# Optimization experiments

Hardware: AMD Instinct MI355X
Metric: run time of the kernel (lower is better)

The kernel has to match this reference:

```python
import jax, jax.numpy as jnp
import numpy as np

B, S, D = 2, 1024, 512
E, K = 8, 2          # num_experts, top_k (hardcoded in EncoderLayerMOE)
HMOE = 4             # SMoE_MHA heads
HD = D // HMOE       # 128 head dim for local experts
HID = 4 * D          # 2048 expert hidden (both extractors)
AH = 4               # attention heads
DK = D // AH
NEG = -1e9


def layer_norm(x, w, b, eps=1e-12):
    mu = x.mean(-1, keepdims=True)
    var = ((x - mu) ** 2).mean(-1, keepdims=True)
    return (x - mu) * jax.lax.rsqrt(var + eps) * w + b


def moe(x, gate_w, gate_b, w1, b1, w2, b2):
    """Dense all-expert SMoE, gather top-k, re-softmax topk weights (faithful).
    x: [..., d]; w1: [E,d,H]; w2: [E,H,d]."""
    gate_scores = x @ gate_w + gate_b                      # [..., E]
    sm = jax.nn.softmax(gate_scores, axis=-1)
    topk_s, topk_i = jax.lax.top_k(sm, K)                  # [..., K]
    h1 = jax.nn.relu(jnp.einsum('...d,edh->...eh', x, w1) + b1)   # [..., E, H]
    out = jnp.einsum('...eh,ehd->...ed', h1, w2) + b2      # [..., E, d]
    idx = jnp.broadcast_to(topk_i[..., None], topk_i.shape + (out.shape[-1],))
    sel = jnp.take_along_axis(out, idx, axis=-2)           # [..., K, d]
    w = jax.nn.softmax(topk_s, axis=-1)[..., None]         # re-softmax of topk scores
    return (sel * w).sum(-2)


def local_extractor(x, pre_w, pre_b, gate_w, gate_b, w1, b1, w2, b2, align_w, align_b):
    b, s, d = x.shape
    xp = x @ pre_w + pre_b
    xf = xp.reshape(b, s, HMOE, HD).transpose(0, 2, 1, 3)  # [b,h,s,hd]
    eo = moe(xf, gate_w, gate_b, w1, b1, w2, b2)
    xf = xf + eo
    xo = xf.transpose(0, 2, 1, 3).reshape(b, s, d)
    return xo @ align_w + align_b


def mha(xq, xkv, mask, wq, bq, wk, bk, wv, bv, wo, bo):
    b, sq, d = xq.shape
    sk = xkv.shape[1]
    q = (xq @ wq + bq).reshape(b, sq, AH, DK).transpose(0, 2, 1, 3)
    k = (xkv @ wk + bk).reshape(b, sk, AH, DK).transpose(0, 2, 1, 3)
    v = (xkv @ wv + bv).reshape(b, sk, AH, DK).transpose(0, 2, 1, 3)
    scores = jnp.einsum('bhqd,bhkd->bhqk', q, k) / jnp.sqrt(jnp.float32(DK))
    m = mask[:, None, :, :]                                 # [b,1,1,sk]
    scores = jnp.where(m, scores, NEG)
    attn = jax.nn.softmax(scores, axis=-1)
    attn = jnp.where(m, attn, 0.0)
    o = jnp.einsum('bhqk,bhkd->bhqd', attn, v)
    o = o.transpose(0, 2, 1, 3).reshape(b, sq, d)
    return o @ wo + bo


def setup_inputs() -> dict:
    key = jax.random.key(0)
    ks = iter(jax.random.split(key, 64))
    def p(shape, scale=0.02):
        return (jax.random.normal(next(ks), shape, jnp.float32) * scale)
    z = lambda *s: jnp.zeros(s, jnp.float32)
    o = lambda *s: jnp.ones(s, jnp.float32)
    return dict(
        x=jax.random.normal(next(ks), (B, S, D), jnp.float32),
        pre_w=p((D, D)), pre_b=z(D),
        l_gate_w=p((HD, E)), l_gate_b=z(E),
        l_w1=p((E, HD, HID)), l_b1=z(E, HID),
        l_w2=p((E, HID, HD)), l_b2=z(E, HD),
        align_w=p((D, D)), align_b=z(D),
        ln1_w=o(D), ln1_b=z(D),
        wq=p((D, D)), bq=z(D), wk=p((D, D)), bk=z(D),
        wv=p((D, D)), bv=z(D), wo=p((D, D)), bo=z(D),
        ln2_w=o(D), ln2_b=z(D),
        g_gate_w=p((D, E)), g_gate_b=z(E),
        g_w1=p((E, D, HID)), g_b1=z(E, HID),
        g_w2=p((E, HID, D)), g_b2=z(E, D),
        mask=jnp.ones((B, 1, S), bool),
    )


def reference(x, pre_w, pre_b, l_gate_w, l_gate_b, l_w1, l_b1, l_w2, l_b2,
              align_w, align_b, ln1_w, ln1_b, wq, bq, wk, bk, wv, bv, wo, bo,
              ln2_w, ln2_b, g_gate_w, g_gate_b, g_w1, g_b1, g_w2, g_b2, mask):
    # EncoderLayerMOE.forward, eval mode, normalize_before=True, cache=None
    residual = x
    xl = local_extractor(x, pre_w, pre_b, l_gate_w, l_gate_b,
                         l_w1, l_b1, l_w2, l_b2, align_w, align_b)
    xn = layer_norm(xl, ln1_w, ln1_b)
    att = mha(xn, xn, mask, wq, bq, wk, bk, wv, bv, wo, bo)
    x1 = residual + att
    residual = x1
    x2 = layer_norm(x1, ln2_w, ln2_b)
    g = moe(x2, g_gate_w, g_gate_b, g_w1, g_b1, g_w2, g_b2)
    out = residual + g
    return out
```

## Files before the change

kernel.cpp:

```cpp
#include <hip/hip_runtime.h>

typedef unsigned short ushort_t;
typedef __attribute__((ext_vector_type(8))) short short8;
typedef __attribute__((ext_vector_type(4))) short short4v;
typedef __attribute__((ext_vector_type(4))) float f32x4;

constexpr int B_    = 2;
constexpr int S_    = 1024;
constexpr int D_    = 512;
constexpr int E_    = 8;
constexpr int HMOE_ = 4;
constexpr int HD_   = 128;
constexpr int HID_  = 2048;
constexpr int AH_   = 4;
constexpr int NTOK  = B_ * S_;
constexpr int NSUB  = B_ * HMOE_ * S_;

#define DEVINL __device__ __forceinline__

DEVINL ushort_t f2bf(float f) {
    union { float f; unsigned int i; } c;
    c.f = f;
    unsigned int x = c.i;
    return (ushort_t)((x + 0x7fffu + ((x >> 16) & 1u)) >> 16);
// ... 296 lines not shown
    #pragma unroll
    for (int j = 0; j < 16; j++) {
        int cc = rl * 16 + j;
        dst[(size_t)cc * R + cl] = f2bf(tile[cl][cc]);
    }
}

struct WCItem { const float* src; ushort_t* dst; int R, C, nbx, nby, start; };
struct WCAll  { WCItem it[10]; };

__global__ __launch_bounds__(256) void wconv_all_k(WCAll a)
{
    __shared__ float tile[64][65];
    const int bidx = blockIdx.x;
    int i = 0;
    #pragma unroll
    for (int j = 1; j < 10; j++) if (bidx >= a.it[j].start) i = j;
    const WCItem wit = a.it[i];
    const int local = bidx - wit.start;
    const int bx = local % wit.nbx;
    const int rest = local / wit.nbx;
    const int by = rest % wit.nby;
    const int e  = rest / wit.nby;
    const int R = wit.R, C = wit.C;
    const int c0 = bx * 64, r0 = by * 64;
    const float* src = wit.src + ((size_t)e * R + r0) * C + c0;
    const int cl = threadIdx.x & 63, rl = threadIdx.x >> 6;
    #pragma unroll
    for (int j = 0; j < 16; j++) {
        int rr = rl * 16 + j;
        tile[rr][cl] = src[(size_t)rr * C + cl];
    }
    __syncthreads();
    ushort_t* dst = wit.dst + ((size_t)e * C + c0) * R + r0;
    #pragma unroll
    for (int j = 0; j < 16; j++) {
        int cc = rl * 16 + j;
        dst[(size_t)cc * R + cl] = f2bf(tile[cl][cc]);
    }
}

__global__ __launch_bounds__(256) void vtrans_bf_k(
    const ushort_t* __restrict__ Vbf, ushort_t* __restrict__ VT)
{
    __shared__ ushort_t tile[64][68];
    const int s0 = blockIdx.x * 64;
    const int d0 = blockIdx.y * 64;
    const int bh = blockIdx.z;
    const int b = bh >> 2, h = bh & 3;
    const ushort_t* src = Vbf + (size_t)(b * S_ + s0) * D_ + h * HD_ + d0;
    const int cl = threadIdx.x & 63, rl = threadIdx.x >> 6;
    #pragma unroll
    for (int j = 0; j < 16; j++) {
        int rr = rl * 16 + j;
        tile[rr][cl] = src[(size_t)rr * D_ + cl];
    }
    __syncthreads();
    ushort_t* dst = VT + ((size_t)bh * HD_ + d0) * S_ + s0;
    #pragma unroll
    for (int j = 0; j < 16; j++) {
        int cc = rl * 16 + j;
        dst[(size_t)cc * S_ + cl] = tile[cl][cc];
    }
}

template <bool LOCAL>
__global__ __launch_bounds__(256) void gate_score_k(
    const float* __restrict__ X, const float* __restrict__ gwm,
    const float* __restrict__ gb, int2* __restrict__ choice,
    float2* __restrict__ cweight)
{
    constexpr int DIMD = LOCAL ? HD_ : D_;
    constexpr int PL = DIMD / 64;
    const int t = blockIdx.x * 4 + (threadIdx.x >> 6);
    const int lane = threadIdx.x & 63;
    const float* x = X + (LOCAL ? local_off(t) : (size_t)t * D_);
    float xr[PL];
    #pragma unroll
    for (int i = 0; i < PL; i++) xr[i] = x[lane + 64 * i];
    float sc[8];
    #pragma unroll
    for (int e = 0; e < 8; e++) {
        float a = 0.f;
        #pragma unroll
        for (int i = 0; i < PL; i++)
            a = fmaf(xr[i], gwm[(size_t)(lane + 64 * i) * E_ + e], a);
        #pragma unroll
        for (int o2 = 32; o2; o2 >>= 1) a += __shfl_xor(a, o2);
        sc[e] = a;
    }
    if (lane == 0) {
        float mx = -1e30f;
        #pragma unroll
        for (int e = 0; e < 8; e++) { sc[e] += gb[e]; mx = fmaxf(mx, sc[e]); }
        float p[8], psum = 0.f;
        #pragma unroll
        for (int e = 0; e < 8; e++) { p[e] = expf(sc[e] - mx); psum += p[e]; }
        float inv = 1.f / psum;
        #pragma unroll
        for (int e = 0; e < 8; e++) p[e] *= inv;
        int i0 = 0;
        for (int e = 1; e < 8; e++) if (p[e] > p[i0]) i0 = e;
        int i1 = (i0 == 0) ? 1 : 0;
        for (int e = 0; e < 8; e++) if (e != i0 && p[e] > p[i1]) i1 = e;
        float e0 = expf(p[i0]), e1 = expf(p[i1]);
        float wnorm = 1.f / (e0 + e1);
        choice[t]  = (int2){i0, i1};
        cweight[t] = (float2){e0 * wnorm, e1 * wnorm};
    }
}

template <int CAP>
__global__ __launch_bounds__(256) void gate_build_k(
    const int2* __restrict__ choice, const float2* __restrict__ cweight,
    int* __restrict__ cnt, int* __restrict__ idx, float* __restrict__ gwv)
{
    __shared__ int wtot[4];
    __shared__ int basesh;
    const int e = blockIdx.x;
    const int tid = threadIdx.x;
    const int lane = tid & 63, wv = tid >> 6;
    if (tid == 0) basesh = 0;
    __syncthreads();
    for (int t0 = 0; t0 < CAP; t0 += 256) {
        int t = t0 + tid;
        int2 ch = choice[t];
        float2 cw = cweight[t];
        bool m0 = (ch.x == e);
        bool m = m0 | (ch.y == e);
        float w = m0 ? cw.x : cw.y;
        unsigned long long mask = __ballot(m);
        int posw = __popcll(mask & ((1ull << lane) - 1ull));
        if (lane == 0) wtot[wv] = __popcll(mask);
        __syncthreads();
        int base = basesh;
        int woff = 0, tot = 0;
        #pragma unroll
        for (int i = 0; i < 4; i++) {
            int c = wtot[i];
            tot += c;
            if (i < wv) woff += c;
        }
        if (m) {
            int p = base + woff + posw;
            idx[e * CAP + p] = t;
            gwv[e * CAP + p] = w;
        }
        __syncthreads();
        if (tid == 0) basesh = base + tot;
    }
    __syncthreads();
    int total = basesh;
    if (tid == 0) cnt[e] = total;
    int padEnd = (total + 63) & ~63;
    if (padEnd > CAP) padEnd = CAP;
    for (int p = total + tid; p < padEnd; p += 256) {
        idx[e * CAP + p] = 0;
        gwv[e * CAP + p] = 0.f;
    }
}

template <int DIMD, int GSPLIT>
__global__ __launch_bounds__(256, 3) void ffn_grouped3_k(
    const ushort_t* __restrict__ Xbf,
    const ushort_t* __restrict__ w1t, const float* __restrict__ b1,
    const ushort_t* __restrict__ w2t, const float* __restrict__ b2,
    const int* __restrict__ cnt, const int* __restrict__ idx,
    const float* __restrict__ gwv, float* __restrict__ OUT)
{
    constexpr int K1  = DIMD;
    constexpr int NT2 = DIMD / 128;
    constexpr int CAP = (DIMD == HD_) ? NSUB : NTOK;
    constexpr int HC  = 128;
    constexpr int CHUNKS = HID_ / HC / GSPLIT;
    constexpr bool PIPE = (NT2 == 1);

    __shared__ ushort_t bufA[64 * 72];
    __shared__ ushort_t bufB[128 * 72];
    __shared__ ushort_t Hs[64 * 136];
    __shared__ float    gws[64];
    __shared__ size_t   toffs[64];

    const int tid  = threadIdx.x;
    const int lane = tid & 63;
    const int wv   = tid >> 6;
    const int e    = blockIdx.x & 7;
    const int rest = blockIdx.x >> 3;
    const int mt   = rest / GSPLIT;
    const int g    = rest % GSPLIT;
    const int m0   = mt * 64;

    if (m0 >= cnt[e]) return;

    if (tid < 64) {
        int t = idx[e * CAP + m0 + tid];
        toffs[tid] = (DIMD == HD_) ? local_off(t) : (size_t)t * D_;
        gws[tid]   = gwv[e * CAP + m0 + tid];
    }
    __syncthreads();

    const int l15 = lane & 15, l4 = lane >> 4;
    const int ar = tid >> 2, as = (tid & 3) * 16;
    const int bn = tid >> 1, bs = (tid & 1) * 32;

    f32x4 accO[NT2][4][2];
    #pragma unroll
    for (int n2 = 0; n2 < NT2; n2++)
        #pragma unroll
        for (int mi = 0; mi < 4; mi++)
            #pragma unroll
            for (int ni = 0; ni < 2; ni++)
                accO[n2][mi][ni] = (f32x4){0.f, 0.f, 0.f, 0.f};

    const ushort_t* w1e = w1t + (size_t)e * HID_ * K1;
    const ushort_t* w2e = w2t + (size_t)e * DIMD * HID_;
    const float* b1e = b1 + (size_t)e * HID_;

    short8 ra0, ra1, rb0, rb1, rb2, rb3;

    const int hc0 = g * CHUNKS * HC;
    for (int hc = hc0; hc < hc0 + CHUNKS * HC; hc += HC) {
        f32x4 acc1[4][2];
        #pragma unroll
        for (int mi = 0; mi < 4; mi++)
            #pragma unroll
            for (int ni = 0; ni < 2; ni++)
                acc1[mi][ni] = (f32x4){0.f, 0.f, 0.f, 0.f};

        if (PIPE) {
            const ushort_t* xp = Xbf + toffs[ar] + as;
            ra0 = *reinterpret_cast<const short8*>(xp);
            ra1 = *reinterpret_cast<const short8*>(xp + 8);
            const ushort_t* wp = w1e + (size_t)(hc + bn) * K1 + bs;
            rb0 = *reinterpret_cast<const short8*>(wp);
            rb1 = *reinterpret_cast<const short8*>(wp + 8);
            rb2 = *reinterpret_cast<const short8*>(wp + 16);
            rb3 = *reinterpret_cast<const short8*>(wp + 24);
        }

        for (int k0 = 0; k0 < K1; k0 += 64) {
            __syncthreads();
            if (PIPE) {
                ushort_t* dst = &bufA[ar * 72 + as];
                *reinterpret_cast<short8*>(dst)     = ra0;
                *reinterpret_cast<short8*>(dst + 8) = ra1;
                ushort_t* dstb = &bufB[bn * 72 + bs];
                *reinterpret_cast<short8*>(dstb)      = rb0;
                *reinterpret_cast<short8*>(dstb + 8)  = rb1;
                *reinterpret_cast<short8*>(dstb + 16) = rb2;
                *reinterpret_cast<short8*>(dstb + 24) = rb3;
                if (k0 + 64 < K1) {
                    const ushort_t* xp = Xbf + toffs[ar] + k0 + 64 + as;
                    ra0 = *reinterpret_cast<const short8*>(xp);
                    ra1 = *reinterpret_cast<const short8*>(xp + 8);
                    const ushort_t* wp = w1e + (size_t)(hc + bn) * K1 + k0 + 64 + bs;
                    rb0 = *reinterpret_cast<const short8*>(wp);
                    rb1 = *reinterpret_cast<const short8*>(wp + 8);
                    rb2 = *reinterpret_cast<const short8*>(wp + 16);
                    rb3 = *reinterpret_cast<const short8*>(wp + 24);
                }
            } else {
                {
                    const ushort_t* xp = Xbf + toffs[ar] + k0 + as;
                    ushort_t* dst = &bufA[ar * 72 + as];
                    *reinterpret_cast<short8*>(dst)     = *reinterpret_cast<const short8*>(xp);
                    *reinterpret_cast<short8*>(dst + 8) = *reinterpret_cast<const short8*>(xp + 8);
                }
                {
                    const ushort_t* wp = w1e + (size_t)(hc + bn) * K1 + k0 + bs;
                    ushort_t* dst = &bufB[bn * 72 + bs];
                    #pragma unroll
                    for (int j = 0; j < 32; j += 8)
                        *reinterpret_cast<short8*>(dst + j) = *reinterpret_cast<const short8*>(wp + j);
                }
            }
            __syncthreads();
            #pragma unroll
            for (int ks = 0; ks < 2; ks++) {
                short8 af[4], bfr[2];
                #pragma unroll
                for (int mi = 0; mi < 4; mi++)
                    af[mi] = *reinterpret_cast<const short8*>(&bufA[(mi * 16 + l15) * 72 + ks * 32 + l4 * 8]);
                #pragma unroll
                for (int ni = 0; ni < 2; ni++)
                    bfr[ni] = *reinterpret_cast<const short8*>(&bufB[(wv * 32 + ni * 16 + l15) * 72 + ks * 32 + l4 * 8]);
                #pragma unroll
                for (int mi = 0; mi < 4; mi++)
                    #pragma unroll
                    for (int ni = 0; ni < 2; ni++)
                        acc1[mi][ni] = __builtin_amdgcn_mfma_f32_16x16x32_bf16(
                            af[mi], bfr[ni], acc1[mi][ni], 0, 0, 0);
            }
        }

        if (PIPE) {
            const ushort_t* wp = w2e + (size_t)bn * HID_ + hc + bs;
            rb0 = *reinterpret_cast<const short8*>(wp);
            rb1 = *reinterpret_cast<const short8*>(wp + 8);
            rb2 = *reinterpret_cast<const short8*>(wp + 16);
            rb3 = *reinterpret_cast<const short8*>(wp + 24);
        }

        float b1v0 = b1e[hc + wv * 32 + l15];
        float b1v1 = b1e[hc + wv * 32 + 16 + l15];
        #pragma unroll
        for (int mi = 0; mi < 4; mi++)
            #pragma unroll
            for (int ni = 0; ni < 2; ni++) {
                float bb = (ni == 0) ? b1v0 : b1v1;
                #pragma unroll
                for (int r = 0; r < 4; r++) {
                    int row = mi * 16 + l4 * 4 + r;
                    int col = wv * 32 + ni * 16 + l15;
                    Hs[row * 136 + col] = f2bf(fmaxf(acc1[mi][ni][r] + bb, 0.f));
                }
            }

        #pragma unroll
        for (int n2 = 0; n2 < NT2; n2++) {
            #pragma unroll
            for (int k2t = 0; k2t < 2; k2t++) {
                __syncthreads();
                if (PIPE) {
                    ushort_t* dst = &bufB[bn * 72 + bs];
                    *reinterpret_cast<short8*>(dst)      = rb0;
                    *reinterpret_cast<short8*>(dst + 8)  = rb1;
                    *reinterpret_cast<short8*>(dst + 16) = rb2;
                    *reinterpret_cast<short8*>(dst + 24) = rb3;
                    if (!(n2 == NT2 - 1 && k2t == 1)) {
                        int nn2 = (k2t == 1) ? n2 + 1 : n2;
                        int nk  = (k2t == 1) ? 0 : 1;
                        const ushort_t* wp = w2e + (size_t)(nn2 * 128 + bn) * HID_ + hc + nk * 64 + bs;
                        rb0 = *reinterpret_cast<const short8*>(wp);
                        rb1 = *reinterpret_cast<const short8*>(wp + 8);
                        rb2 = *reinterpret_cast<const short8*>(wp + 16);
                        rb3 = *reinterpret_cast<const short8*>(wp + 24);
                    }
                } else {
                    const ushort_t* wp = w2e + (size_t)(n2 * 128 + bn) * HID_ + hc + k2t * 64 + bs;
                    ushort_t* dst = &bufB[bn * 72 + bs];
                    #pragma unroll
                    for (int j = 0; j < 32; j += 8)
                        *reinterpret_cast<short8*>(dst + j) = *reinterpret_cast<const short8*>(wp + j);
                }
                __syncthreads();
                #pragma unroll
                for (int ks = 0; ks < 2; ks++) {
                    short8 af[4], bfr[2];
                    #pragma unroll
                    for (int mi = 0; mi < 4; mi++)
                        af[mi] = *reinterpret_cast<const short8*>(&Hs[(mi * 16 + l15) * 136 + k2t * 64 + ks * 32 + l4 * 8]);
                    #pragma unroll
                    for (int ni = 0; ni < 2; ni++)
                        bfr[ni] = *reinterpret_cast<const short8*>(&bufB[(wv * 32 + ni * 16 + l15) * 72 + ks * 32 + l4 * 8]);
                    #pragma unroll
                    for (int mi = 0; mi < 4; mi++)
                        #pragma unroll
                        for (int ni = 0; ni < 2; ni++)
                            accO[n2][mi][ni] = __builtin_amdgcn_mfma_f32_16x16x32_bf16(
                                af[mi], bfr[ni], accO[n2][mi][ni], 0, 0, 0);
                }
            }
        }
    }

    #pragma unroll
    for (int n2 = 0; n2 < NT2; n2++) {
        float b2v0 = (g == 0) ? b2[(size_t)e * DIMD + n2 * 128 + wv * 32 + l15] : 0.f;
        float b2v1 = (g == 0) ? b2[(size_t)e * DIMD + n2 * 128 + wv * 32 + 16 + l15] : 0.f;
        #pragma unroll
        for (int mi = 0; mi < 4; mi++)
            #pragma unroll
            for (int r = 0; r < 4; r++) {
                int row = mi * 16 + l4 * 4 + r;
                float gg = gws[row];
                if (gg != 0.f) {
                    float* op = OUT + toffs[row] + n2 * 128 + wv * 32;
                    atomicAdd(op + l15,      gg * (accO[n2][mi][0][r] + b2v0));
                    atomicAdd(op + 16 + l15, gg * (accO[n2][mi][1][r] + b2v1));
                }
            }
    }
}

__global__ __launch_bounds__(256) void ffn1g_k(
    const ushort_t* __restrict__ Xbf,
    const ushort_t* __restrict__ w1t, const float* __restrict__ b1,
    const int* __restrict__ cnt, const int* __restrict__ idx,
    int hbase, ushort_t* __restrict__ Hbuf)
{
    __shared__ ushort_t bufA[64 * 72];
    __shared__ ushort_t bufB[128 * 72];
    __shared__ size_t   toffs[64];
    __shared__ int      sbase;

    const int tid  = threadIdx.x;
    const int lane = tid & 63;
    const int wv   = tid >> 6;
    const int e    = blockIdx.x & 7;
    const int rest = blockIdx.x >> 3;
    const int mt   = rest >> 3;
    const int hs   = rest & 7;
    const int m0   = mt * 64;
    const int ce   = cnt[e];
    if (m0 >= ce) return;

    if (tid < 64) toffs[tid] = (size_t)idx[e * NTOK + m0 + tid] * D_;
    if (tid == 0) {
        int s = 0;
        for (int j = 0; j < e; j++) s += cnt[j];
        sbase = s;
    }
    __syncthreads();

    const int l15 = lane & 15, l4 = lane >> 4;
    const int ar = tid >> 2, as = (tid & 3) * 16;
    const int bn = tid >> 1, bs = (tid & 1) * 32;
    const int hc = hbase + hs * 128;

    const ushort_t* w1e = w1t + (size_t)e * HID_ * D_;

    f32x4 acc1[4][2];
    #pragma unroll
    for (int mi = 0; mi < 4; mi++)
        #pragma unroll
        for (int ni = 0; ni < 2; ni++)
            acc1[mi][ni] = (f32x4){0.f, 0.f, 0.f, 0.f};

    short8 ra0, ra1, rb0, rb1, rb2, rb3;
    {
        const ushort_t* xp = Xbf + toffs[ar] + as;
        ra0 = *reinterpret_cast<const short8*>(xp);
        ra1 = *reinterpret_cast<const short8*>(xp + 8);
        const ushort_t* wp = w1e + (size_t)(hc + bn) * D_ + bs;
        rb0 = *reinterpret_cast<const short8*>(wp);
        rb1 = *reinterpret_cast<const short8*>(wp + 8);
        rb2 = *reinterpret_cast<const short8*>(wp + 16);
        rb3 = *reinterpret_cast<const short8*>(wp + 24);
    }
    for (int k0 = 0; k0 < D_; k0 += 64) {
        __syncthreads();
        {
            ushort_t* dst = &bufA[ar * 72 + as];
            *reinterpret_cast<short8*>(dst)     = ra0;
            *reinterpret_cast<short8*>(dst + 8) = ra1;
            ushort_t* dstb = &bufB[bn * 72 + bs];
            *reinterpret_cast<short8*>(dstb)      = rb0;
            *reinterpret_cast<short8*>(dstb + 8)  = rb1;
            *reinterpret_cast<short8*>(dstb + 16) = rb2;
            *reinterpret_cast<short8*>(dstb + 24) = rb3;
        }
        if (k0 + 64 < D_) {
            const ushort_t* xp = Xbf + toffs[ar] + k0 + 64 + as;
            ra0 = *reinterpret_cast<const short8*>(xp);
            ra1 = *reinterpret_cast<const short8*>(xp + 8);
            const ushort_t* wp = w1e + (size_t)(hc + bn) * D_ + k0 + 64 + bs;
            rb0 = *reinterpret_cast<const short8*>(wp);
            rb1 = *reinterpret_cast<const short8*>(wp + 8);
            rb2 = *reinterpret_cast<const short8*>(wp + 16);
            rb3 = *reinterpret_cast<const short8*>(wp + 24);
        }
        __syncthreads();
        #pragma unroll
        for (int ks = 0; ks < 2; ks++) {
            short8 af[4], bfr[2];
            #pragma unroll
            for (int mi = 0; mi < 4; mi++)
                af[mi] = *reinterpret_cast<const short8*>(&bufA[(mi * 16 + l15) * 72 + ks * 32 + l4 * 8]);
            #pragma unroll
            for (int ni = 0; ni < 2; ni++)
                bfr[ni] = *reinterpret_cast<const short8*>(&bufB[(wv * 32 + ni * 16 + l15) * 72 + ks * 32 + l4 * 8]);
            #pragma unroll
            for (int mi = 0; mi < 4; mi++)
                #pragma unroll
                for (int ni = 0; ni < 2; ni++)
                    acc1[mi][ni] = __builtin_amdgcn_mfma_f32_16x16x32_bf16(
                        af[mi], bfr[ni], acc1[mi][ni], 0, 0, 0);
        }
    }

    const int slotbase = sbase + m0;
    const int hout = (hc - hbase);
    float b1v0 = b1[(size_t)e * HID_ + hc + wv * 32 + l15];
    float b1v1 = b1[(size_t)e * HID_ + hc + wv * 32 + 16 + l15];
    #pragma unroll
    for (int mi = 0; mi < 4; mi++)
        #pragma unroll
        for (int ni = 0; ni < 2; ni++) {
            float bb = (ni == 0) ? b1v0 : b1v1;
            #pragma unroll
            for (int r = 0; r < 4; r++) {
                int row = mi * 16 + l4 * 4 + r;
                if (m0 + row < ce) {
                    int col = hout + wv * 32 + ni * 16 + l15;
                    Hbuf[(size_t)(slotbase + row) * 1024 + col] =
                        f2bf(fmaxf(acc1[mi][ni][r] + bb, 0.f));
                }
            }
        }
}

template <bool ADD_B2>
__global__ __launch_bounds__(256) void ffn2g_k(
    const ushort_t* __restrict__ Hbuf,
    const ushort_t* __restrict__ w2t, const float* __restrict__ b2,
    const int* __restrict__ cnt, const int* __restrict__ idx,
    const float* __restrict__ gwv, int hbase, float* __restrict__ OUT)
{
    __shared__ ushort_t bufA[32 * 72];
    __shared__ ushort_t bufB[128 * 72];
    __shared__ float    gws[32];
    __shared__ size_t   toffs[32];
    __shared__ int      sbase;

    const int tid  = threadIdx.x;
    const int lane = tid & 63;
    const int wv   = tid >> 6;
    const int e    = blockIdx.x & 7;
    const int rest = blockIdx.x >> 3;
    const int mt   = rest >> 2;
    const int n2   = rest & 3;
    const int m0   = mt * 32;
    const int ce   = cnt[e];
    if (m0 >= ce) return;

    if (tid < 32) {
        toffs[tid] = (size_t)idx[e * NTOK + m0 + tid] * D_;
        gws[tid]   = gwv[e * NTOK + m0 + tid];
    }
    if (tid == 0) {
        int s = 0;
        for (int j = 0; j < e; j++) s += cnt[j];
        sbase = s;
    }
    __syncthreads();
// ... 469 lines not shown
            sum += __shfl_xor(sum, 1);
            sum += __shfl_xor(sum, 2);
            sum += __shfl_xor(sum, 4);
            if ((tid & 7) == 0) { mrow[r] = mnew; lrow[r] = lrow[r] * alpha + sum; arow[r] = alpha; }
        }
        __syncthreads();

        {
            #pragma unroll
            for (int i2 = 0; i2 < 4; i2++) {
                float al = arow[py * 4 + i2];
                #pragma unroll
                for (int j = 0; j < 4; j++) o[i2][j] *= al;
            }
            #pragma unroll 4
            for (int k = 0; k < KC; k++) {
                float4 pv = *reinterpret_cast<const float4*>(&psT[k][py * 4]);
                float4 vv = *reinterpret_cast<const float4*>(V + base + (size_t)(kc + k) * D_ + px * 4);
                float pa[4] = {pv.x, pv.y, pv.z, pv.w};
                #pragma unroll
                for (int i2 = 0; i2 < 4; i2++) {
                    o[i2][0] = fmaf(pa[i2], vv.x, o[i2][0]);
                    o[i2][1] = fmaf(pa[i2], vv.y, o[i2][1]);
                    o[i2][2] = fmaf(pa[i2], vv.z, o[i2][2]);
                    o[i2][3] = fmaf(pa[i2], vv.w, o[i2][3]);
                }
            }
        }
        __syncthreads();
    }

    #pragma unroll
    for (int i2 = 0; i2 < 4; i2++) {
        float inv = 1.f / lrow[py * 4 + i2];
        float4 ov;
        ov.x = o[i2][0] * inv; ov.y = o[i2][1] * inv;
        ov.z = o[i2][2] * inv; ov.w = o[i2][3] * inv;
        *reinterpret_cast<float4*>(AO + base + (size_t)(q0 + py * 4 + i2) * D_ + px * 4) = ov;
    }
}

__global__ __launch_bounds__(256) void copy_out_k(
    const float* __restrict__ X, float* __restrict__ Y, int n)
{
    int base = (blockIdx.x * 256 + threadIdx.x) * 4;
    if (base < n)
        *reinterpret_cast<float4*>(Y + base) = *reinterpret_cast<const float4*>(X + base);
}

extern "C" void kernel_launch(void* const* d_in, const int* in_sizes, int n_in,
                              void* d_out, int out_size, void* d_ws, size_t ws_size,
                              hipStream_t stream)
{
    (void)in_sizes; (void)n_in; (void)out_size;
    const float* x        = (const float*)d_in[0];
    const float* pre_w    = (const float*)d_in[1];
    const float* pre_b    = (const float*)d_in[2];
    const float* l_gate_w = (const float*)d_in[3];
    const float* l_gate_b = (const float*)d_in[4];
    const float* l_w1     = (const float*)d_in[5];
    const float* l_b1     = (const float*)d_in[6];
    const float* l_w2     = (const float*)d_in[7];
    const float* l_b2     = (const float*)d_in[8];
    const float* align_w  = (const float*)d_in[9];
    const float* align_b  = (const float*)d_in[10];
    const float* ln1_w    = (const float*)d_in[11];
    const float* ln1_b    = (const float*)d_in[12];
    const float* wq       = (const float*)d_in[13];
    const float* bq       = (const float*)d_in[14];
    const float* wk       = (const float*)d_in[15];
    const float* bk       = (const float*)d_in[16];
    const float* wv       = (const float*)d_in[17];
    const float* bv       = (const float*)d_in[18];
    const float* wo       = (const float*)d_in[19];
    const float* bo       = (const float*)d_in[20];
    const float* ln2_w    = (const float*)d_in[21];
    const float* ln2_b    = (const float*)d_in[22];
    const float* g_gate_w = (const float*)d_in[23];
    const float* g_gate_b = (const float*)d_in[24];
    const float* g_w1     = (const float*)d_in[25];
    const float* g_b1     = (const float*)d_in[26];
    const float* g_w2     = (const float*)d_in[27];
    const float* g_b2     = (const float*)d_in[28];

    char* ws = (char*)d_ws;
    const size_t MB  = 1024 * 1024;
    const size_t MB4 = (size_t)NTOK * D_ * sizeof(float);
    float* W0 = (float*)(ws + 0 * MB);
    float* W1 = (float*)(ws + 4 * MB);
    float* W2 = (float*)(ws + 8 * MB);

    const bool pre = ws_size >= (size_t)59 * MB;

    char* blob = ws + (pre ? 12 : 16) * MB;
    int*    cntl = (int*)(blob);
    int*    cntg = (int*)(blob + 32);
    int*    idxl = (int*)(blob + 64);
    int*    idxg = (int*)(blob + 64 + 262144);
    float*  gwvl = (float*)(blob + 64 + 262144 + 65536);
    float*  gwvg = (float*)(blob + 64 + 262144 + 65536 + 262144);
    int2*   chl  = (int2*)(blob + 64 + 262144 + 65536 + 262144 + 65536);
    float2* cwl  = (float2*)((char*)chl + 65536);
    int2*   chg  = (int2*)((char*)cwl + 65536);
    float2* cwg  = (float2*)((char*)chg + 16384);

    ushort_t* preT   = (ushort_t*)(ws + 14 * MB);
    ushort_t* alignT = (ushort_t*)(ws + 14 * MB + 512 * 1024);
    ushort_t* wqT    = (ushort_t*)(ws + 15 * MB);
    ushort_t* wkT    = (ushort_t*)(ws + 15 * MB + 512 * 1024);
    ushort_t* wvT    = (ushort_t*)(ws + 16 * MB);
    ushort_t* woT    = (ushort_t*)(ws + 16 * MB + 512 * 1024);
    ushort_t* XBF  = (ushort_t*)(ws + 17 * MB);
    ushort_t* Vbf  = (ushort_t*)(ws + 4 * MB);
    ushort_t* VTb  = (ushort_t*)(ws + 6 * MB);
    ushort_t* Qbf  = (ushort_t*)(ws + 8 * MB);
    ushort_t* Kbf  = (ushort_t*)(ws + 10 * MB);
    ushort_t* Hbuf = (ushort_t*)(ws + 4 * MB);
    ushort_t* LW1T = (ushort_t*)(ws + 19 * MB);
    ushort_t* LW2T = (ushort_t*)(ws + 23 * MB);
    ushort_t* GW1T = (ushort_t*)(ws + 27 * MB);
    ushort_t* GW2T = (ushort_t*)(ws + 43 * MB);
    float* W3 = (float*)(ws + 12 * MB);

    const dim3 gg(D_ / 64, NTOK / 64);
    const dim3 gg32(D_ / 64, NTOK / 32);

    if (pre) {
        {
            WCAll a;
            auto set = [&](int i, const float* s, ushort_t* d, int R, int C,
                           int E, int start) {
                a.it[i].src = s; a.it[i].dst = d; a.it[i].R = R; a.it[i].C = C;
                a.it[i].nbx = C / 64; a.it[i].nby = R / 64; a.it[i].start = start;
                return start + (C / 64) * (R / 64) * E;
            };
            int st = 0;
            st = set(0, pre_w,   preT,   D_,   D_,   1, st);
            st = set(1, align_w, alignT, D_,   D_,   1, st);
            st = set(2, wq,      wqT,    D_,   D_,   1, st);
            st = set(3, wk,      wkT,    D_,   D_,   1, st);
            st = set(4, wv,      wvT,    D_,   D_,   1, st);
            st = set(5, wo,      woT,    D_,   D_,   1, st);
            st = set(6, l_w1,    LW1T,   HD_,  HID_, 8, st);
            st = set(7, l_w2,    LW2T,   HID_, HD_,  8, st);
            st = set(8, g_w1,    GW1T,   D_,   HID_, 8, st);
            st = set(9, g_w2,    GW2T,   HID_, D_,   8, st);
            wconv_all_k<<<st, 256, 0, stream>>>(a);
        }

        gemm_mfma_k<true, true, true, false><<<gg32, 256, 0, stream>>>(
            nullptr, x, preT, pre_b, nullptr, W0, XBF);
        gate_score_k<true><<<NSUB / 4, 256, 0, stream>>>(W0, l_gate_w, l_gate_b, chl, cwl);
        gate_build_k<NSUB><<<8, 256, 0, stream>>>(chl, cwl, cntl, idxl, gwvl);
        ffn_grouped3_k<HD_, 4><<<8 * (NSUB / 64) * 4, 256, 0, stream>>>(
            XBF, LW1T, l_b1, LW2T, l_b2, cntl, idxl, gwvl, W0);
        gemm_mfma_k<true, true, false, false><<<gg32, 256, 0, stream>>>(
            nullptr, W0, alignT, align_b, nullptr, W2, nullptr);
        ln_k<false, true><<<NTOK, 256, 0, stream>>>(W2, ln1_w, ln1_b, W0, XBF);
        {
            QKVW qp;
            qp.wt[0] = wqT; qp.wt[1] = wkT; qp.wt[2] = wvT;
            qp.bias[0] = bq; qp.bias[1] = bk; qp.bias[2] = bv;
            qp.out[0] = Qbf; qp.out[1] = Kbf; qp.out[2] = Vbf;
            gemm_qkv_k<<<dim3(24, 64), 256, 0, stream>>>(XBF, qp);
        }
        vtrans_bf_k<<<dim3(16, 2, 8), 256, 0, stream>>>(Vbf, VTb);
        fattn_mfma_k<<<dim3(S_ / 32, B_ * AH_), 256, 0, stream>>>(Qbf, Kbf, VTb, XBF);
        gemm_mfma_k<false, true, false, true><<<gg32, 256, 0, stream>>>(
            XBF, nullptr, woT, bo, x, (float*)d_out, nullptr);
        ln_gate_k<<<NTOK, 256, 0, stream>>>(
            (const float*)d_out, ln2_w, ln2_b, XBF, g_gate_w, g_gate_b, chg, cwg);
        gate_build_k<NTOK><<<8, 256, 0, stream>>>(chg, cwg, cntg, idxg, gwvg);
        ffn1g_k<<<8 * 32 * 8, 256, 0, stream>>>(
            XBF, GW1T, g_b1, cntg, idxg, 0, Hbuf);
        ffn2g_k<true><<<8 * 64 * 4, 256, 0, stream>>>(
            Hbuf, GW2T, g_b2, cntg, idxg, gwvg, 0, (float*)d_out);
        ffn1g_k<<<8 * 32 * 8, 256, 0, stream>>>(
            XBF, GW1T, g_b1, cntg, idxg, 1024, Hbuf);
        ffn2g_k<false><<<8 * 64 * 4, 256, 0, stream>>>(
            Hbuf, GW2T, g_b2, cntg, idxg, gwvg, 1024, (float*)d_out);
    } else {
        gemm_bias_k<false><<<gg, 256, 0, stream>>>(x, pre_w, pre_b, nullptr, W0, NTOK, D_, D_);
        gate_score_k<true><<<NSUB / 4, 256, 0, stream>>>(W0, l_gate_w, l_gate_b, chl, cwl);
        gate_build_k<NSUB><<<8, 256, 0, stream>>>(chl, cwl, cntl, idxl, gwvl);
        hipMemcpyAsync(W1, W0, MB4, hipMemcpyDeviceToDevice, stream);
        ffn_grouped_k<HD_><<<8 * (NSUB / 64), 256, 0, stream>>>(
            W0, l_w1, l_b1, l_w2, l_b2, cntl, idxl, gwvl, W1);
        gemm_bias_k<false><<<gg, 256, 0, stream>>>(W1, align_w, align_b, nullptr, W2, NTOK, D_, D_);
        ln_k<true, false><<<NTOK, 256, 0, stream>>>(W2, ln1_w, ln1_b, W0, nullptr);
        gemm_bias_k<false><<<gg, 256, 0, stream>>>(W0, wq, bq, nullptr, W1, NTOK, D_, D_);
        gemm_bias_k<false><<<gg, 256, 0, stream>>>(W0, wk, bk, nullptr, W2, NTOK, D_, D_);
        gemm_bias_k<false><<<gg, 256, 0, stream>>>(W0, wv, bv, nullptr, W3, NTOK, D_, D_);
        fattn_k<<<dim3(S_ / QT, B_ * AH_), 256, 0, stream>>>(W1, W2, W3, W1);
        gemm_bias_k<true><<<gg, 256, 0, stream>>>(W1, wo, bo, x, W0, NTOK, D_, D_);
        ln_k<true, false><<<NTOK, 256, 0, stream>>>(W0, ln2_w, ln2_b, W2, nullptr);
        gate_score_k<false><<<NTOK / 4, 256, 0, stream>>>(W2, g_gate_w, g_gate_b, chg, cwg);
        gate_build_k<NTOK><<<8, 256, 0, stream>>>(chg, cwg, cntg, idxg, gwvg);
        ffn_grouped_k<D_><<<8 * (NTOK / 64) * 4, 256, 0, stream>>>(
            W2, g_w1, g_b1, g_w2, g_b2, cntg, idxg, gwvg, W0);
        copy_out_k<<<(NTOK * D_) / (256 * 4), 256, 0, stream>>>(W0, (float*)d_out, NTOK * D_);
    }
}
```

Baseline: 428.7 us.

## Double token tile to 128 rows in local expert grouped FFN kernel

Specialises the grouped expert FFN kernel for the local (head-dim 128) path and raises the token tile per block from 64 to 128 rows, so each expert weight tile loaded into shared memory serves twice as many tokens. Routing padding is raised to multiples of 128 to match. The W2 prefetch is folded into the last K1 iteration so it overlaps the first GEMM. In exchange the kernel uses more LDS and accumulator registers, occupancy is lowered to 2 blocks per SM, and the grid halves, which may leave fewer blocks in flight and add more padded rows for small experts.

```diff
diff --git a/kernel.cpp b/kernel.cpp
--- a/kernel.cpp
+++ b/kernel.cpp
@@ -472,7 +472,7 @@
     __syncthreads();
     int total = basesh;
     if (tid == 0) cnt[e] = total;
-    int padEnd = (total + 63) & ~63;
+    int padEnd = (total + 127) & ~127;
     if (padEnd > CAP) padEnd = CAP;
     for (int p = total + tid; p < padEnd; p += 256) {
         idx[e * CAP + p] = 0;
@@ -480,26 +480,24 @@
     }
 }
 
-template <int DIMD, int GSPLIT>
-__global__ __launch_bounds__(256, 3) void ffn_grouped3_k(
+template <int GSPLIT>
+__global__ __launch_bounds__(256, 2) void ffn_local5_k(
     const ushort_t* __restrict__ Xbf,
     const ushort_t* __restrict__ w1t, const float* __restrict__ b1,
     const ushort_t* __restrict__ w2t, const float* __restrict__ b2,
     const int* __restrict__ cnt, const int* __restrict__ idx,
     const float* __restrict__ gwv, float* __restrict__ OUT)
 {
-    constexpr int K1  = DIMD;
-    constexpr int NT2 = DIMD / 128;
-    constexpr int CAP = (DIMD == HD_) ? NSUB : NTOK;
-    constexpr int HC  = 128;
+    constexpr int K1 = HD_;
+    constexpr int CAP = NSUB;
+    constexpr int HC = 128;
     constexpr int CHUNKS = HID_ / HC / GSPLIT;
-    constexpr bool PIPE = (NT2 == 1);
-
-    __shared__ ushort_t bufA[64 * 72];
+
+    __shared__ ushort_t bufA[128 * 72];
     __shared__ ushort_t bufB[128 * 72];
-    __shared__ ushort_t Hs[64 * 136];
-    __shared__ float    gws[64];
-    __shared__ size_t   toffs[64];
+    __shared__ ushort_t Hs[128 * 136];
+    __shared__ float    gws[128];
+    __shared__ size_t   toffs[128];
 
     const int tid  = threadIdx.x;
     const int lane = tid & 63;
@@ -508,49 +506,49 @@
     const int rest = blockIdx.x >> 3;
     const int mt   = rest / GSPLIT;
     const int g    = rest % GSPLIT;
-    const int m0   = mt * 64;
+    const int m0   = mt * 128;
 
     if (m0 >= cnt[e]) return;
 
-    if (tid < 64) {
+    if (tid < 128) {
         int t = idx[e * CAP + m0 + tid];
-        toffs[tid] = (DIMD == HD_) ? local_off(t) : (size_t)t * D_;
+        toffs[tid] = local_off(t);
         gws[tid]   = gwv[e * CAP + m0 + tid];
     }
     __syncthreads();
 
     const int l15 = lane & 15, l4 = lane >> 4;
-    const int ar = tid >> 2, as = (tid & 3) * 16;
+    const int ar = tid >> 1, aseg = (tid & 1) * 32;
     const int bn = tid >> 1, bs = (tid & 1) * 32;
 
-    f32x4 accO[NT2][4][2];
-    #pragma unroll
-    for (int n2 = 0; n2 < NT2; n2++)
-        #pragma unroll
-        for (int mi = 0; mi < 4; mi++)
-            #pragma unroll
-            for (int ni = 0; ni < 2; ni++)
-                accO[n2][mi][ni] = (f32x4){0.f, 0.f, 0.f, 0.f};
+    f32x4 accO[8][2];
+    #pragma unroll
+    for (int mi = 0; mi < 8; mi++)
+        #pragma unroll
+        for (int ni = 0; ni < 2; ni++)
+            accO[mi][ni] = (f32x4){0.f, 0.f, 0.f, 0.f};
 
     const ushort_t* w1e = w1t + (size_t)e * HID_ * K1;
-    const ushort_t* w2e = w2t + (size_t)e * DIMD * HID_;
+    const ushort_t* w2e = w2t + (size_t)e * HD_ * HID_;
     const float* b1e = b1 + (size_t)e * HID_;
 
-    short8 ra0, ra1, rb0, rb1, rb2, rb3;
+    short8 ra0, ra1, ra2, ra3, rb0, rb1, rb2, rb3;
 
     const int hc0 = g * CHUNKS * HC;
     for (int hc = hc0; hc < hc0 + CHUNKS * HC; hc += HC) {
-        f32x4 acc1[4][2];
-        #pragma unroll
-        for (int mi = 0; mi < 4; mi++)
+        f32x4 acc1[8][2];
+        #pragma unroll
+        for (int mi = 0; mi < 8; mi++)
             #pragma unroll
             for (int ni = 0; ni < 2; ni++)
                 acc1[mi][ni] = (f32x4){0.f, 0.f, 0.f, 0.f};
 
-        if (PIPE) {
-            const ushort_t* xp = Xbf + toffs[ar] + as;
+        {
+            const ushort_t* xp = Xbf + toffs[ar] + aseg;
             ra0 = *reinterpret_cast<const short8*>(xp);
             ra1 = *reinterpret_cast<const short8*>(xp + 8);
+            ra2 = *reinterpret_cast<const short8*>(xp + 16);
+            ra3 = *reinterpret_cast<const short8*>(xp + 24);
             const ushort_t* wp = w1e + (size_t)(hc + bn) * K1 + bs;
             rb0 = *reinterpret_cast<const short8*>(wp);
             rb1 = *reinterpret_cast<const short8*>(wp + 8);
@@ -558,73 +556,61 @@
             rb3 = *reinterpret_cast<const short8*>(wp + 24);
         }
 
+        #pragma unroll
         for (int k0 = 0; k0 < K1; k0 += 64) {
             __syncthreads();
-            if (PIPE) {
-                ushort_t* dst = &bufA[ar * 72 + as];
-                *reinterpret_cast<short8*>(dst)     = ra0;
-                *reinterpret_cast<short8*>(dst + 8) = ra1;
+            {
+                ushort_t* dst = &bufA[ar * 72 + aseg];
+                *reinterpret_cast<short8*>(dst)      = ra0;
+                *reinterpret_cast<short8*>(dst + 8)  = ra1;
+                *reinterpret_cast<short8*>(dst + 16) = ra2;
+                *reinterpret_cast<short8*>(dst + 24) = ra3;
                 ushort_t* dstb = &bufB[bn * 72 + bs];
                 *reinterpret_cast<short8*>(dstb)      = rb0;
                 *reinterpret_cast<short8*>(dstb + 8)  = rb1;
                 *reinterpret_cast<short8*>(dstb + 16) = rb2;
                 *reinterpret_cast<short8*>(dstb + 24) = rb3;
-                if (k0 + 64 < K1) {
-                    const ushort_t* xp = Xbf + toffs[ar] + k0 + 64 + as;
-                    ra0 = *reinterpret_cast<const short8*>(xp);
-                    ra1 = *reinterpret_cast<const short8*>(xp + 8);
-                    const ushort_t* wp = w1e + (size_t)(hc + bn) * K1 + k0 + 64 + bs;
-                    rb0 = *reinterpret_cast<const short8*>(wp);
-                    rb1 = *reinterpret_cast<const short8*>(wp + 8);
-                    rb2 = *reinterpret_cast<const short8*>(wp + 16);
-                    rb3 = *reinterpret_cast<const short8*>(wp + 24);
-                }
+            }
+            if (k0 + 64 < K1) {
+                const ushort_t* xp = Xbf + toffs[ar] + k0 + 64 + aseg;
+                ra0 = *reinterpret_cast<const short8*>(xp);
+                ra1 = *reinterpret_cast<const short8*>(xp + 8);
+                ra2 = *reinterpret_cast<const short8*>(xp + 16);
+                ra3 = *reinterpret_cast<const short8*>(xp + 24);
+                const ushort_t* wp = w1e + (size_t)(hc + bn) * K1 + k0 + 64 + bs;
+                rb0 = *reinterpret_cast<const short8*>(wp);
+                rb1 = *reinterpret_cast<const short8*>(wp + 8);
+                rb2 = *reinterpret_cast<const short8*>(wp + 16);
+                rb3 = *reinterpret_cast<const short8*>(wp + 24);
             } else {
-                {
-                    const ushort_t* xp = Xbf + toffs[ar] + k0 + as;
-                    ushort_t* dst = &bufA[ar * 72 + as];
-                    *reinterpret_cast<short8*>(dst)     = *reinterpret_cast<const short8*>(xp);
-                    *reinterpret_cast<short8*>(dst + 8) = *reinterpret_cast<const short8*>(xp + 8);
-                }
-                {
-                    const ushort_t* wp = w1e + (size_t)(hc + bn) * K1 + k0 + bs;
-                    ushort_t* dst = &bufB[bn * 72 + bs];
-                    #pragma unroll
-                    for (int j = 0; j < 32; j += 8)
-                        *reinterpret_cast<short8*>(dst + j) = *reinterpret_cast<const short8*>(wp + j);
-                }
+                const ushort_t* wp = w2e + (size_t)bn * HID_ + hc + bs;
+                rb0 = *reinterpret_cast<const short8*>(wp);
+                rb1 = *reinterpret_cast<const short8*>(wp + 8);
+                rb2 = *reinterpret_cast<const short8*>(wp + 16);
+                rb3 = *reinterpret_cast<const short8*>(wp + 24);
             }
             __syncthreads();
             #pragma unroll
             for (int ks = 0; ks < 2; ks++) {
-                short8 af[4], bfr[2];
-                #pragma unroll
-                for (int mi = 0; mi < 4; mi++)
-                    af[mi] = *reinterpret_cast<const short8*>(&bufA[(mi * 16 + l15) * 72 + ks * 32 + l4 * 8]);
+                short8 bfr[2];
                 #pragma unroll
                 for (int ni = 0; ni < 2; ni++)
                     bfr[ni] = *reinterpret_cast<const short8*>(&bufB[(wv * 32 + ni * 16 + l15) * 72 + ks * 32 + l4 * 8]);
                 #pragma unroll
-                for (int mi = 0; mi < 4; mi++)
+                for (int mi = 0; mi < 8; mi++) {
+                    short8 af = *reinterpret_cast<const short8*>(&bufA[(mi * 16 + l15) * 72 + ks * 32 + l4 * 8]);
                     #pragma unroll
                     for (int ni = 0; ni < 2; ni++)
                         acc1[mi][ni] = __builtin_amdgcn_mfma_f32_16x16x32_bf16(
-                            af[mi], bfr[ni], acc1[mi][ni], 0, 0, 0);
-            }
-        }
-
-        if (PIPE) {
-            const ushort_t* wp = w2e + (size_t)bn * HID_ + hc + bs;
-            rb0 = *reinterpret_cast<const short8*>(wp);
-            rb1 = *reinterpret_cast<const short8*>(wp + 8);
-            rb2 = *reinterpret_cast<const short8*>(wp + 16);
-            rb3 = *reinterpret_cast<const short8*>(wp + 24);
+                            af, bfr[ni], acc1[mi][ni], 0, 0, 0);
+                }
+            }
         }
 
         float b1v0 = b1e[hc + wv * 32 + l15];
         float b1v1 = b1e[hc + wv * 32 + 16 + l15];
         #pragma unroll
-        for (int mi = 0; mi < 4; mi++)
+        for (int mi = 0; mi < 8; mi++)
             #pragma unroll
             for (int ni = 0; ni < 2; ni++) {
                 float bb = (ni == 0) ? b1v0 : b1v1;
@@ -637,70 +623,55 @@
             }
 
         #pragma unroll
-        for (int n2 = 0; n2 < NT2; n2++) {
-            #pragma unroll
-            for (int k2t = 0; k2t < 2; k2t++) {
-                __syncthreads();
-                if (PIPE) {
-                    ushort_t* dst = &bufB[bn * 72 + bs];
-                    *reinterpret_cast<short8*>(dst)      = rb0;
-                    *reinterpret_cast<short8*>(dst + 8)  = rb1;
-                    *reinterpret_cast<short8*>(dst + 16) = rb2;
-                    *reinterpret_cast<short8*>(dst + 24) = rb3;
-                    if (!(n2 == NT2 - 1 && k2t == 1)) {
-                        int nn2 = (k2t == 1) ? n2 + 1 : n2;
-                        int nk  = (k2t == 1) ? 0 : 1;
-                        const ushort_t* wp = w2e + (size_t)(nn2 * 128 + bn) * HID_ + hc + nk * 64 + bs;
-                        rb0 = *reinterpret_cast<const short8*>(wp);
-                        rb1 = *reinterpret_cast<const short8*>(wp + 8);
-                        rb2 = *reinterpret_cast<const short8*>(wp + 16);
-                        rb3 = *reinterpret_cast<const short8*>(wp + 24);
-                    }
-                } else {
-                    const ushort_t* wp = w2e + (size_t)(n2 * 128 + bn) * HID_ + hc + k2t * 64 + bs;
-                    ushort_t* dst = &bufB[bn * 72 + bs];
-                    #pragma unroll
-                    for (int j = 0; j < 32; j += 8)
-                        *reinterpret_cast<short8*>(dst + j) = *reinterpret_cast<const short8*>(wp + j);
-                }
-                __syncthreads();
-                #pragma unroll
-                for (int ks = 0; ks < 2; ks++) {
-                    short8 af[4], bfr[2];
-                    #pragma unroll
-                    for (int mi = 0; mi < 4; mi++)
-                        af[mi] = *reinterpret_cast<const short8*>(&Hs[(mi * 16 + l15) * 136 + k2t * 64 + ks * 32 + l4 * 8]);
+        for (int k2t = 0; k2t < 2; k2t++) {
+            __syncthreads();
+            {
+                ushort_t* dstb = &bufB[bn * 72 + bs];
+                *reinterpret_cast<short8*>(dstb)      = rb0;
+                *reinterpret_cast<short8*>(dstb + 8)  = rb1;
+                *reinterpret_cast<short8*>(dstb + 16) = rb2;
+                *reinterpret_cast<short8*>(dstb + 24) = rb3;
+            }
+            if (k2t == 0) {
+                const ushort_t* wp = w2e + (size_t)bn * HID_ + hc + 64 + bs;
+                rb0 = *reinterpret_cast<const short8*>(wp);
+                rb1 = *reinterpret_cast<const short8*>(wp + 8);
+                rb2 = *reinterpret_cast<const short8*>(wp + 16);
+                rb3 = *reinterpret_cast<const short8*>(wp + 24);
+            }
+            __syncthreads();
+            #pragma unroll
+            for (int ks = 0; ks < 2; ks++) {
+                short8 bfr[2];
+                #pragma unroll
+                for (int ni = 0; ni < 2; ni++)
+                    bfr[ni] = *reinterpret_cast<const short8*>(&bufB[(wv * 32 + ni * 16 + l15) * 72 + ks * 32 + l4 * 8]);
+                #pragma unroll
+                for (int mi = 0; mi < 8; mi++) {
+                    short8 af = *reinterpret_cast<const short8*>(&Hs[(mi * 16 + l15) * 136 + k2t * 64 + ks * 32 + l4 * 8]);
                     #pragma unroll
                     for (int ni = 0; ni < 2; ni++)
-                        bfr[ni] = *reinterpret_cast<const short8*>(&bufB[(wv * 32 + ni * 16 + l15) * 72 + ks * 32 + l4 * 8]);
-                    #pragma unroll
-                    for (int mi = 0; mi < 4; mi++)
-                        #pragma unroll
-                        for (int ni = 0; ni < 2; ni++)
-                            accO[n2][mi][ni] = __builtin_amdgcn_mfma_f32_16x16x32_bf16(
-                                af[mi], bfr[ni], accO[n2][mi][ni], 0, 0, 0);
+                        accO[mi][ni] = __builtin_amdgcn_mfma_f32_16x16x32_bf16(
+                            af, bfr[ni], accO[mi][ni], 0, 0, 0);
                 }
             }
         }
     }
 
-    #pragma unroll
-    for (int n2 = 0; n2 < NT2; n2++) {
-        float b2v0 = (g == 0) ? b2[(size_t)e * DIMD + n2 * 128 + wv * 32 + l15] : 0.f;
-        float b2v1 = (g == 0) ? b2[(size_t)e * DIMD + n2 * 128 + wv * 32 + 16 + l15] : 0.f;
-        #pragma unroll
-        for (int mi = 0; mi < 4; mi++)
-            #pragma unroll
-            for (int r = 0; r < 4; r++) {
-                int row = mi * 16 + l4 * 4 + r;
-                float gg = gws[row];
-                if (gg != 0.f) {
-                    float* op = OUT + toffs[row] + n2 * 128 + wv * 32;
-                    atomicAdd(op + l15,      gg * (accO[n2][mi][0][r] + b2v0));
-                    atomicAdd(op + 16 + l15, gg * (accO[n2][mi][1][r] + b2v1));
-                }
-            }
-    }
+    float b2v0 = (g == 0) ? b2[(size_t)e * HD_ + wv * 32 + l15] : 0.f;
+    float b2v1 = (g == 0) ? b2[(size_t)e * HD_ + wv * 32 + 16 + l15] : 0.f;
+    #pragma unroll
+    for (int mi = 0; mi < 8; mi++)
+        #pragma unroll
+        for (int r = 0; r < 4; r++) {
+            int row = mi * 16 + l4 * 4 + r;
+            float gg = gws[row];
+            if (gg != 0.f) {
+                float* op = OUT + toffs[row] + wv * 32;
+                atomicAdd(op + l15,      gg * (accO[mi][0][r] + b2v0));
+                atomicAdd(op + 16 + l15, gg * (accO[mi][1][r] + b2v1));
+            }
+        }
 }
 
 __global__ __launch_bounds__(256) void ffn1g_k(
@@ -1476,7 +1447,7 @@
             nullptr, x, preT, pre_b, nullptr, W0, XBF);
         gate_score_k<true><<<NSUB / 4, 256, 0, stream>>>(W0, l_gate_w, l_gate_b, chl, cwl);
         gate_build_k<NSUB><<<8, 256, 0, stream>>>(chl, cwl, cntl, idxl, gwvl);
-        ffn_grouped3_k<HD_, 4><<<8 * (NSUB / 64) * 4, 256, 0, stream>>>(
+        ffn_local5_k<4><<<8 * (NSUB / 128) * 4, 256, 0, stream>>>(
             XBF, LW1T, l_b1, LW2T, l_b2, cntl, idxl, gwvl, W0);
         gemm_mfma_k<true, true, false, false><<<gg32, 256, 0, stream>>>(
             nullptr, W0, alignT, align_b, nullptr, W2, nullptr);
```

Result: slower. 447.6 us (+4.4%).
